# Optimization experiments

Hardware: AMD Instinct MI355X
Metric: run time of the kernel (lower is better)

Reference implementation:

```python
import jax, jax.numpy as jnp
import numpy as np

N_SPEAKERS, N_UTTER, EMB_DIM = 1024, 20, 256


def setup_inputs() -> dict:
    key = jax.random.key(0)
    k_in, = jax.random.split(key, 1)
    inp = jax.random.normal(k_in, (N_SPEAKERS, N_UTTER, EMB_DIM), dtype=jnp.float32)
    w = jnp.asarray(10.0, dtype=jnp.float32)
    b = jnp.asarray(-5.0, dtype=jnp.float32)
    return {"input": inp, "w": w, "b": b}


def reference(input, w, b):
    # input: [N, M, D] utterance embeddings
    N, M, D = input.shape
    centroids = jnp.mean(input, axis=1)                       # [N, D]
    # leave-one-out centroid for each (speaker, utterance):
    # mean of the other M-1 utterances of the same speaker
    excl = (centroids[:, None, :] * M - input) / (M - 1)      # [N, M, D]

    inv_u = 1.0 / jnp.linalg.norm(input, axis=-1, keepdims=True)      # [N, M, 1]
    u_hat = input * inv_u                                             # [N, M, D]
    c_hat = centroids / jnp.linalg.norm(centroids, axis=-1, keepdims=True)  # [N, D]
    e_hat = excl / jnp.linalg.norm(excl, axis=-1, keepdims=True)      # [N, M, D]

    # cosine sim of every utterance vs every full centroid
    cs = jnp.einsum('nmd,kd->nmk', u_hat, c_hat)              # [N, M, N]
    # override k == own speaker with the excluded-centroid cosine
    cs_self = jnp.sum(u_hat * e_hat, axis=-1)                 # [N, M]
    idx = jnp.arange(N)
    cs = cs.at[idx, :, idx].set(cs_self)

    sim = w * cs + b                                          # scaled similarity
    logp = jax.nn.log_softmax(sim, axis=-1)                   # softmax over speakers
    loss = -jnp.sum(logp[idx, :, idx])
    return loss
```

## Files before the change

### kernel.cpp

```cpp
#include <hip/hip_runtime.h>
#include <hip/hip_fp8.h>


#define D_DIM 256
#define N_SPK 1024
#define M_UTT 20

typedef long lx2 __attribute__((ext_vector_type(2)));
typedef float f32x16 __attribute__((ext_vector_type(16)));

__device__ __forceinline__ int pk4_fp8(float x0, float x1, float x2, float x3) {
#if __has_builtin(__builtin_amdgcn_cvt_pk_fp8_f32)
  int v = __builtin_amdgcn_cvt_pk_fp8_f32(x0, x1, 0, false);
  v = __builtin_amdgcn_cvt_pk_fp8_f32(x2, x3, v, true);
  return v;
#else
  union { int i; unsigned char b[4]; } u;
  u.b[0] = __hip_fp8_e4m3(x0).__x;
  u.b[1] = __hip_fp8_e4m3(x1).__x;
  u.b[2] = __hip_fp8_e4m3(x2).__x;
  u.b[3] = __hip_fp8_e4m3(x3).__x;
  return u.i;
#endif
}

__global__ __launch_bounds__(256) void ge2e_prep(
    const float* __restrict__ inp, unsigned int* __restrict__ bsw32,
    float* __restrict__ c_raw, float* __restrict__ ccv,
    float* __restrict__ out) {
  const int tid = threadIdx.x, lane = tid & 63, wv = tid >> 6;
  const int s = blockIdx.x * 4 + wv;
  if (blockIdx.x == 0 && tid == 0) out[0] = 0.0f;

  const float4* up =
      reinterpret_cast<const float4*>(inp + (size_t)s * (M_UTT * D_DIM)) + lane;
  float4 a = make_float4(0.f, 0.f, 0.f, 0.f);
#pragma unroll
  for (int m = 0; m < M_UTT; ++m) {
    const float4 f = up[m * (D_DIM / 4)];
    a.x += f.x; a.y += f.y; a.z += f.z; a.w += f.w;
  }
  const float inv = 1.0f / (float)M_UTT;
  const float4 c = make_float4(a.x * inv, a.y * inv, a.z * inv, a.w * inv);
  reinterpret_cast<float4*>(c_raw + (size_t)s * D_DIM)[lane] = c;

  float cc = c.x * c.x + c.y * c.y + c.z * c.z + c.w * c.w;
#pragma unroll
  for (int o = 1; o < 64; o <<= 1) cc += __shfl_xor(cc, o, 64);
  if (lane == 0) ccv[s] = cc;

  const float r = rsqrtf(fmaxf(cc, 1e-20f));
  const int q = pk4_fp8(c.x * r, c.y * r, c.z * r, c.w * r);
  const int t = s >> 5, n5 = s & 31;
  const int p = lane >> 3, sub = (lane >> 2) & 1;
  const int half = (lane >> 1) & 1, jb = (lane & 1) * 4;
  bsw32[((((t * 8 + p) * 64) + half * 32 + n5) * 16 + sub * 8 + jb) >> 2] =
      (unsigned int)q;
}

__global__ __launch_bounds__(256) void ge2e_main(
    const float* __restrict__ inp, const float* __restrict__ wp,
    const unsigned char* __restrict__ bsw, const float* __restrict__ c_raw,
    const float* __restrict__ ccv, float* __restrict__ out) {
  __shared__ __align__(16) unsigned char lA[32 * D_DIM];
  __shared__ float uuL[32], ucL[32], ccL[32];
  __shared__ float rowtot[4][32];
  const int tid = threadIdx.x;
  const int r0 = blockIdx.x * 32;
  const float w = wp[0];

  {
    const int m = tid >> 3, seg = tid & 7;
    const int r = r0 + m, nr = r / M_UTT;
    const float4* urow =
        reinterpret_cast<const float4*>(inp + (size_t)r * D_DIM + seg * 32);
    const float4* crow =
        reinterpret_cast<const float4*>(c_raw + (size_t)nr * D_DIM + seg * 32);
    float4 uf[8];
    float uu = 0.f, uc = 0.f;
#pragma unroll
    for (int q = 0; q < 8; ++q) {
      uf[q] = urow[q];
      const float4 cf = crow[q];
      uu += uf[q].x * uf[q].x + uf[q].y * uf[q].y + uf[q].z * uf[q].z +
            uf[q].w * uf[q].w;
      uc += uf[q].x * cf.x + uf[q].y * cf.y + uf[q].z * cf.z + uf[q].w * cf.w;
    }
#pragma unroll
    for (int o = 1; o < 8; o <<= 1) {
      uu += __shfl_xor(uu, o, 64);
      uc += __shfl_xor(uc, o, 64);
    }
    const float s = w * rsqrtf(fmaxf(uu, 1e-20f));
    int4 ch0, ch1;
    ch0.x = pk4_fp8(s * uf[0].x, s * uf[0].y, s * uf[0].z, s * uf[0].w);
    ch0.y = pk4_fp8(s * uf[1].x, s * uf[1].y, s * uf[1].z, s * uf[1].w);
    ch0.z = pk4_fp8(s * uf[4].x, s * uf[4].y, s * uf[4].z, s * uf[4].w);
    ch0.w = pk4_fp8(s * uf[5].x, s * uf[5].y, s * uf[5].z, s * uf[5].w);
    ch1.x = pk4_fp8(s * uf[2].x, s * uf[2].y, s * uf[2].z, s * uf[2].w);
    ch1.y = pk4_fp8(s * uf[3].x, s * uf[3].y, s * uf[3].z, s * uf[3].w);
    ch1.z = pk4_fp8(s * uf[6].x, s * uf[6].y, s * uf[6].z, s * uf[6].w);
    ch1.w = pk4_fp8(s * uf[7].x, s * uf[7].y, s * uf[7].z, s * uf[7].w);
    reinterpret_cast<int4*>(lA)[seg * 64 + m] = ch0;
    reinterpret_cast<int4*>(lA)[seg * 64 + m + 32] = ch1;
    if (seg == 0) {
      uuL[m] = uu;
      ucL[m] = uc;
      ccL[m] = ccv[nr];
    }
  }
  __syncthreads();

  const int lane = tid & 63, wv = tid >> 6, hl = lane >> 5;
  lx2 A[8];
  const lx2* lAv = reinterpret_cast<const lx2*>(lA);
#pragma unroll
  for (int p = 0; p < 8; ++p) A[p] = lAv[p * 64 + lane];

  float sume[16];
#pragma unroll
  for (int i = 0; i < 16; ++i) sume[i] = 0.0f;

  const lx2* Bv = reinterpret_cast<const lx2*>(bsw);
#pragma unroll 1
  for (int t = 0; t < 8; ++t) {
    const lx2* Bt = Bv + (size_t)(wv * 8 + t) * 512 + lane;
    lx2 B[8];
#pragma unroll
    for (int p = 0; p < 8; ++p) B[p] = Bt[p * 64];
    f32x16 acc0, acc1;
#pragma unroll
    for (int i = 0; i < 16; ++i) { acc0[i] = 0.0f; acc1[i] = 0.0f; }
#pragma unroll
    for (int p = 0; p < 8; ++p) {
      acc0 = __builtin_amdgcn_mfma_f32_32x32x16_fp8_fp8(A[p].x, B[p].x, acc0,
                                                        0, 0, 0);
      acc1 = __builtin_amdgcn_mfma_f32_32x32x16_fp8_fp8(A[p].y, B[p].y, acc1,
                                                        0, 0, 0);
    }
#pragma unroll
    for (int i = 0; i < 16; ++i)
      sume[i] += __expf(fminf(acc0[i] + acc1[i], 40.0f));
  }

#pragma unroll
  for (int i = 0; i < 16; ++i) {
    float v = sume[i];
#pragma unroll
    for (int o = 1; o < 32; o <<= 1) v += __shfl_xor(v, o, 64);
    sume[i] = v;
  }
  if ((lane & 31) == 0) {
#pragma unroll
    for (int i = 0; i < 16; ++i)
      rowtot[wv][(i & 3) + 8 * (i >> 2) + 4 * hl] = sume[i];
  }
  __syncthreads();

  if (tid < 32) {
    const float se0 = rowtot[0][tid] + rowtot[1][tid] + rowtot[2][tid] +
                      rowtot[3][tid];
    const float uu = uuL[tid], uc = ucL[tid], cc = ccL[tid];
    const float Mf = (float)M_UTT;
    const float ue = (Mf * uc - uu) * (1.0f / (Mf - 1.0f));
    const float ee = (Mf * Mf * cc - 2.0f * Mf * uc + uu) *
                     (1.0f / ((Mf - 1.0f) * (Mf - 1.0f)));
    const float sself = w * ue * rsqrtf(fmaxf(uu * ee, 1e-20f));
    const float sown = w * uc * rsqrtf(fmaxf(uu * cc, 1e-20f));
    const float se = fmaxf(
        se0 + __expf(fminf(sself, 40.f)) - __expf(fminf(sown, 40.f)), 1e-10f);
    float v = __logf(se) - sself;
#pragma unroll
    for (int o = 1; o < 32; o <<= 1) v += __shfl_xor(v, o, 64);
    if (tid == 0) atomicAdd(out, v);
  }
}

extern "C" void kernel_launch(void* const* d_in, const int* in_sizes, int n_in,
                              void* d_out, int out_size, void* d_ws, size_t ws_size,
                              hipStream_t stream) {
  const float* inp = (const float*)d_in[0];
  const float* wp  = (const float*)d_in[1];
  float* out = (float*)d_out;

  unsigned char* bsw = (unsigned char*)d_ws;
  float* c_raw = (float*)((char*)d_ws + 256 * 1024);
  float* ccv   = c_raw + (size_t)N_SPK * D_DIM;

  ge2e_prep<<<N_SPK / 4, 256, 0, stream>>>(inp, (unsigned int*)bsw, c_raw, ccv,
                                           out);
  ge2e_main<<<(N_SPK * M_UTT) / 32, 256, 0, stream>>>(inp, wp, bsw, c_raw, ccv,
                                                      out);
}
```

Before: 90.89 us.

## Quantize utterances to FP8 in prep kernel and double-buffer B loads in main

The prep kernel now keeps each speaker's utterances in registers, computes per-utterance norms and dot products with the centroid, and writes FP8-quantized A fragments in MFMA layout to workspace. The main kernel no longer rereads fp32 input and centroids. It loads pre-swizzled A straight from global memory and software-pipelines the B tile loads with two register buffers, raising MFMA priority and setting launch bounds to three blocks per SIMD. This cuts fp32 traffic in the main kernel, at the cost of more register pressure in prep and an extra workspace round trip.

```diff
diff --git a/kernel.cpp b/kernel.cpp
--- a/kernel.cpp
+++ b/kernel.cpp
@@ -25,123 +25,139 @@
 }
 
 __global__ __launch_bounds__(256) void ge2e_prep(
-    const float* __restrict__ inp, unsigned int* __restrict__ bsw32,
-    float* __restrict__ c_raw, float* __restrict__ ccv,
-    float* __restrict__ out) {
+    const float* __restrict__ inp, const float* __restrict__ wp,
+    unsigned int* __restrict__ bsw32, int4* __restrict__ Ag,
+    float* __restrict__ uuA, float* __restrict__ ucA,
+    float* __restrict__ ccv, float* __restrict__ out) {
+  __shared__ unsigned int q8[4][M_UTT][65];
   const int tid = threadIdx.x, lane = tid & 63, wv = tid >> 6;
   const int s = blockIdx.x * 4 + wv;
   if (blockIdx.x == 0 && tid == 0) out[0] = 0.0f;
 
   const float4* up =
       reinterpret_cast<const float4*>(inp + (size_t)s * (M_UTT * D_DIM)) + lane;
+  float4 uf[M_UTT];
   float4 a = make_float4(0.f, 0.f, 0.f, 0.f);
 #pragma unroll
   for (int m = 0; m < M_UTT; ++m) {
-    const float4 f = up[m * (D_DIM / 4)];
-    a.x += f.x; a.y += f.y; a.z += f.z; a.w += f.w;
+    uf[m] = up[m * (D_DIM / 4)];
+    a.x += uf[m].x; a.y += uf[m].y; a.z += uf[m].z; a.w += uf[m].w;
   }
   const float inv = 1.0f / (float)M_UTT;
   const float4 c = make_float4(a.x * inv, a.y * inv, a.z * inv, a.w * inv);
-  reinterpret_cast<float4*>(c_raw + (size_t)s * D_DIM)[lane] = c;
 
   float cc = c.x * c.x + c.y * c.y + c.z * c.z + c.w * c.w;
 #pragma unroll
   for (int o = 1; o < 64; o <<= 1) cc += __shfl_xor(cc, o, 64);
   if (lane == 0) ccv[s] = cc;
 
-  const float r = rsqrtf(fmaxf(cc, 1e-20f));
-  const int q = pk4_fp8(c.x * r, c.y * r, c.z * r, c.w * r);
-  const int t = s >> 5, n5 = s & 31;
-  const int p = lane >> 3, sub = (lane >> 2) & 1;
-  const int half = (lane >> 1) & 1, jb = (lane & 1) * 4;
-  bsw32[((((t * 8 + p) * 64) + half * 32 + n5) * 16 + sub * 8 + jb) >> 2] =
-      (unsigned int)q;
-}
-
-__global__ __launch_bounds__(256) void ge2e_main(
-    const float* __restrict__ inp, const float* __restrict__ wp,
-    const unsigned char* __restrict__ bsw, const float* __restrict__ c_raw,
-    const float* __restrict__ ccv, float* __restrict__ out) {
-  __shared__ __align__(16) unsigned char lA[32 * D_DIM];
-  __shared__ float uuL[32], ucL[32], ccL[32];
-  __shared__ float rowtot[4][32];
-  const int tid = threadIdx.x;
-  const int r0 = blockIdx.x * 32;
+  {
+    const float rc = rsqrtf(fmaxf(cc, 1e-20f));
+    const int qb = pk4_fp8(c.x * rc, c.y * rc, c.z * rc, c.w * rc);
+    const int t = s >> 5, n5 = s & 31;
+    const int p = lane >> 3, sub = (lane >> 2) & 1;
+    const int hf = (lane >> 1) & 1, jb = (lane & 1) * 4;
+    bsw32[((((t * 8 + p) * 64) + hf * 32 + n5) * 16 + sub * 8 + jb) >> 2] =
+        (unsigned int)qb;
+  }
+
   const float w = wp[0];
-
-  {
-    const int m = tid >> 3, seg = tid & 7;
-    const int r = r0 + m, nr = r / M_UTT;
-    const float4* urow =
-        reinterpret_cast<const float4*>(inp + (size_t)r * D_DIM + seg * 32);
-    const float4* crow =
-        reinterpret_cast<const float4*>(c_raw + (size_t)nr * D_DIM + seg * 32);
-    float4 uf[8];
-    float uu = 0.f, uc = 0.f;
-#pragma unroll
-    for (int q = 0; q < 8; ++q) {
-      uf[q] = urow[q];
-      const float4 cf = crow[q];
-      uu += uf[q].x * uf[q].x + uf[q].y * uf[q].y + uf[q].z * uf[q].z +
-            uf[q].w * uf[q].w;
-      uc += uf[q].x * cf.x + uf[q].y * cf.y + uf[q].z * cf.z + uf[q].w * cf.w;
-    }
-#pragma unroll
-    for (int o = 1; o < 8; o <<= 1) {
+#pragma unroll
+  for (int m = 0; m < M_UTT; ++m) {
+    float uu = uf[m].x * uf[m].x + uf[m].y * uf[m].y + uf[m].z * uf[m].z +
+               uf[m].w * uf[m].w;
+    float uc = uf[m].x * c.x + uf[m].y * c.y + uf[m].z * c.z + uf[m].w * c.w;
+#pragma unroll
+    for (int o = 1; o < 64; o <<= 1) {
       uu += __shfl_xor(uu, o, 64);
       uc += __shfl_xor(uc, o, 64);
     }
-    const float s = w * rsqrtf(fmaxf(uu, 1e-20f));
-    int4 ch0, ch1;
-    ch0.x = pk4_fp8(s * uf[0].x, s * uf[0].y, s * uf[0].z, s * uf[0].w);
-    ch0.y = pk4_fp8(s * uf[1].x, s * uf[1].y, s * uf[1].z, s * uf[1].w);
-    ch0.z = pk4_fp8(s * uf[4].x, s * uf[4].y, s * uf[4].z, s * uf[4].w);
-    ch0.w = pk4_fp8(s * uf[5].x, s * uf[5].y, s * uf[5].z, s * uf[5].w);
-    ch1.x = pk4_fp8(s * uf[2].x, s * uf[2].y, s * uf[2].z, s * uf[2].w);
-    ch1.y = pk4_fp8(s * uf[3].x, s * uf[3].y, s * uf[3].z, s * uf[3].w);
-    ch1.z = pk4_fp8(s * uf[6].x, s * uf[6].y, s * uf[6].z, s * uf[6].w);
-    ch1.w = pk4_fp8(s * uf[7].x, s * uf[7].y, s * uf[7].z, s * uf[7].w);
-    reinterpret_cast<int4*>(lA)[seg * 64 + m] = ch0;
-    reinterpret_cast<int4*>(lA)[seg * 64 + m + 32] = ch1;
-    if (seg == 0) {
-      uuL[m] = uu;
-      ucL[m] = uc;
-      ccL[m] = ccv[nr];
-    }
+    if (lane == 0) {
+      uuA[s * M_UTT + m] = uu;
+      ucA[s * M_UTT + m] = uc;
+    }
+    const float sm = w * rsqrtf(fmaxf(uu, 1e-20f));
+    q8[wv][m][lane] =
+        (unsigned int)pk4_fp8(sm * uf[m].x, sm * uf[m].y, sm * uf[m].z,
+                              sm * uf[m].w);
   }
   __syncthreads();
 
-  const int lane = tid & 63, wv = tid >> 6, hl = lane >> 5;
+  if (lane < 2 * M_UTT) {
+    const int m = lane >> 1, hf = lane & 1;
+    const int r = s * M_UTT + m;
+    const int br = r >> 5, l2 = (r & 31) + 32 * hf;
+#pragma unroll
+    for (int p = 0; p < 8; ++p) {
+      const int c0 = 8 * p + 2 * hf;
+      int4 v;
+      v.x = (int)q8[wv][m][c0];
+      v.y = (int)q8[wv][m][c0 + 1];
+      v.z = (int)q8[wv][m][c0 + 4];
+      v.w = (int)q8[wv][m][c0 + 5];
+      Ag[((size_t)(br * 8 + p)) * 64 + l2] = v;
+    }
+  }
+}
+
+__global__ __launch_bounds__(256, 3) void ge2e_main(
+    const int4* __restrict__ Ag, const unsigned char* __restrict__ bsw,
+    const float* __restrict__ wp, const float* __restrict__ uuA,
+    const float* __restrict__ ucA, const float* __restrict__ ccv,
+    float* __restrict__ out) {
+  __shared__ float rowtot[4][32];
+  const int tid = threadIdx.x, lane = tid & 63, wv = tid >> 6, hl = lane >> 5;
+
   lx2 A[8];
-  const lx2* lAv = reinterpret_cast<const lx2*>(lA);
-#pragma unroll
-  for (int p = 0; p < 8; ++p) A[p] = lAv[p * 64 + lane];
+  const lx2* Agv = reinterpret_cast<const lx2*>(Ag);
+#pragma unroll
+  for (int p = 0; p < 8; ++p)
+    A[p] = Agv[((size_t)blockIdx.x * 8 + p) * 64 + lane];
 
   float sume[16];
 #pragma unroll
   for (int i = 0; i < 16; ++i) sume[i] = 0.0f;
 
-  const lx2* Bv = reinterpret_cast<const lx2*>(bsw);
-#pragma unroll 1
-  for (int t = 0; t < 8; ++t) {
-    const lx2* Bt = Bv + (size_t)(wv * 8 + t) * 512 + lane;
-    lx2 B[8];
-#pragma unroll
-    for (int p = 0; p < 8; ++p) B[p] = Bt[p * 64];
-    f32x16 acc0, acc1;
-#pragma unroll
-    for (int i = 0; i < 16; ++i) { acc0[i] = 0.0f; acc1[i] = 0.0f; }
-#pragma unroll
-    for (int p = 0; p < 8; ++p) {
-      acc0 = __builtin_amdgcn_mfma_f32_32x32x16_fp8_fp8(A[p].x, B[p].x, acc0,
-                                                        0, 0, 0);
-      acc1 = __builtin_amdgcn_mfma_f32_32x32x16_fp8_fp8(A[p].y, B[p].y, acc1,
-                                                        0, 0, 0);
-    }
-#pragma unroll
-    for (int i = 0; i < 16; ++i)
-      sume[i] += __expf(fminf(acc0[i] + acc1[i], 40.0f));
-  }
+  const lx2* Bw = reinterpret_cast<const lx2*>(bsw) + (size_t)wv * 4096 + lane;
+  lx2 Ba[8], Bb[8];
+#pragma unroll
+  for (int p = 0; p < 8; ++p) Ba[p] = Bw[p * 64];
+
+#define ACC_EXP(Bx)                                                          \
+  {                                                                          \
+    f32x16 acc0, acc1;                                                       \
+    _Pragma("unroll") for (int i = 0; i < 16; ++i) {                         \
+      acc0[i] = 0.0f;                                                        \
+      acc1[i] = 0.0f;                                                        \
+    }                                                                        \
+    __builtin_amdgcn_s_setprio(1);                                           \
+    _Pragma("unroll") for (int p = 0; p < 8; ++p) {                          \
+      acc0 = __builtin_amdgcn_mfma_f32_32x32x16_fp8_fp8(A[p].x, Bx[p].x,     \
+                                                        acc0, 0, 0, 0);      \
+      acc1 = __builtin_amdgcn_mfma_f32_32x32x16_fp8_fp8(A[p].y, Bx[p].y,     \
+                                                        acc1, 0, 0, 0);      \
+    }                                                                        \
+    __builtin_amdgcn_s_setprio(0);                                           \
+    _Pragma("unroll") for (int i = 0; i < 16; ++i)                           \
+        sume[i] += __expf(fminf(acc0[i] + acc1[i], 40.0f));      \
+  }
+
+#pragma unroll
+  for (int tt = 0; tt < 4; ++tt) {
+    {
+      const lx2* Bt = Bw + (2 * tt + 1) * 512;
+#pragma unroll
+      for (int p = 0; p < 8; ++p) Bb[p] = Bt[p * 64];
+    }
+    ACC_EXP(Ba);
+    if (tt < 3) {
+      const lx2* Bt = Bw + (2 * tt + 2) * 512;
+#pragma unroll
+      for (int p = 0; p < 8; ++p) Ba[p] = Bt[p * 64];
+    }
+    ACC_EXP(Bb);
+  }
+#undef ACC_EXP
 
 #pragma unroll
   for (int i = 0; i < 16; ++i) {
@@ -158,9 +174,11 @@
   __syncthreads();
 
   if (tid < 32) {
+    const int r = blockIdx.x * 32 + tid;
     const float se0 = rowtot[0][tid] + rowtot[1][tid] + rowtot[2][tid] +
                       rowtot[3][tid];
-    const float uu = uuL[tid], uc = ucL[tid], cc = ccL[tid];
+    const float uu = uuA[r], uc = ucA[r], cc = ccv[r / M_UTT];
+    const float w = wp[0];
     const float Mf = (float)M_UTT;
     const float ue = (Mf * uc - uu) * (1.0f / (Mf - 1.0f));
     const float ee = (Mf * Mf * cc - 2.0f * Mf * uc + uu) *
@@ -184,11 +202,13 @@
   float* out = (float*)d_out;
 
   unsigned char* bsw = (unsigned char*)d_ws;
-  float* c_raw = (float*)((char*)d_ws + 256 * 1024);
-  float* ccv   = c_raw + (size_t)N_SPK * D_DIM;
-
-  ge2e_prep<<<N_SPK / 4, 256, 0, stream>>>(inp, (unsigned int*)bsw, c_raw, ccv,
-                                           out);
-  ge2e_main<<<(N_SPK * M_UTT) / 32, 256, 0, stream>>>(inp, wp, bsw, c_raw, ccv,
-                                                      out);
-}
+  int4* Ag   = (int4*)((char*)d_ws + 256 * 1024);
+  float* uuA = (float*)((char*)d_ws + 256 * 1024 + 5 * 1024 * 1024);
+  float* ucA = uuA + (size_t)N_SPK * M_UTT;
+  float* ccv = ucA + (size_t)N_SPK * M_UTT;
+
+  ge2e_prep<<<N_SPK / 4, 256, 0, stream>>>(inp, wp, (unsigned int*)bsw, Ag,
+                                           uuA, ucA, ccv, out);
+  ge2e_main<<<(N_SPK * M_UTT) / 32, 256, 0, stream>>>(Ag, bsw, wp, uuA, ucA,
+                                                      ccv, out);
+}
```

New measurement: 108.0 us. 1.19x slower.
